# Optimization experiments

Measured on AMD Instinct MI355X. Metric: run time of the kernel, lower is better.

## Reference

```python
import jax, jax.numpy as jnp
import numpy as np

B, T, IN, H, OUT = 32, 1024, 256, 768, 128


def setup_inputs() -> dict:
    key = jax.random.key(0)
    ks = jax.random.split(key, 11)
    s = 0.05
    return {
        "x": jax.random.normal(ks[0], (B, T, IN), dtype=jnp.float32),
        "W_ih0": jax.random.normal(ks[1], (4 * H, IN), dtype=jnp.float32) * s,
        "W_hh0": jax.random.normal(ks[2], (4 * H, H), dtype=jnp.float32) * s,
        "b_ih0": jax.random.normal(ks[3], (4 * H,), dtype=jnp.float32) * s,
        "b_hh0": jax.random.normal(ks[4], (4 * H,), dtype=jnp.float32) * s,
        "W_ih1": jax.random.normal(ks[5], (4 * H, H), dtype=jnp.float32) * s,
        "W_hh1": jax.random.normal(ks[6], (4 * H, H), dtype=jnp.float32) * s,
        "b_ih1": jax.random.normal(ks[7], (4 * H,), dtype=jnp.float32) * s,
        "b_hh1": jax.random.normal(ks[8], (4 * H,), dtype=jnp.float32) * s,
        "W_lin": jax.random.normal(ks[9], (OUT, H), dtype=jnp.float32) * s,
        "b_lin": jax.random.normal(ks[10], (OUT,), dtype=jnp.float32) * s,
    }


def _lstm_layer(x_btd, W_ih, W_hh, b_ih, b_hh):
    # Input-side GEMM for all timesteps at once: [B,T,4H]
    xg = jnp.einsum("btd,gd->btg", x_btd, W_ih) + b_ih + b_hh
    xg = jnp.swapaxes(xg, 0, 1)  # time-major [T,B,4H]
    h0 = jnp.zeros((x_btd.shape[0], W_hh.shape[1]), x_btd.dtype)

    def step(carry, gx):
        h, c = carry
        g = gx + h @ W_hh.T  # [B,4H]
        i, f, gg, o = jnp.split(g, 4, axis=-1)  # PyTorch gate order i,f,g,o
        i, f, o = jax.nn.sigmoid(i), jax.nn.sigmoid(f), jax.nn.sigmoid(o)
        c = f * c + i * jnp.tanh(gg)
        h = o * jnp.tanh(c)
        return (h, c), h

    _, hs = jax.lax.scan(step, (h0, h0), xg)  # hs: [T,B,H]
    return jnp.swapaxes(hs, 0, 1)  # [B,T,H]


def reference(x, W_ih0, W_hh0, b_ih0, b_hh0, W_ih1, W_hh1, b_ih1, b_hh1, W_lin, b_lin):
    h1 = _lstm_layer(x, W_ih0, W_hh0, b_ih0, b_hh0)
    h2 = _lstm_layer(h1, W_ih1, W_hh1, b_ih1, b_hh1)  # eval mode: inter-layer dropout off
    return jnp.einsum("bth,oh->bto", h2, W_lin) + b_lin
```

## Files before the change

### kernel.cpp

```cpp
#include <hip/hip_runtime.h>

#define Tt    1024
#define INF   256
#define Hh    768
#define OUTF  128

#define NWG_L0  48
#define NWG_L1  48
#define NWG_LIN 2
#define NWG     (NWG_L0 + NWG_L1 + NWG_LIN)
#define NTHR    1024

typedef unsigned int       u32;
typedef unsigned long long u64;
typedef unsigned short     u16;
typedef __attribute__((ext_vector_type(8))) short bf16x8;
typedef __attribute__((ext_vector_type(4))) float f32x4;

#define PROG_OFF 0
#define HA_OFF   16384
#define HB_OFF   (HA_OFF + 3*49152)
#define WS_BYTES (HB_OFF + 3*49152)
#define HPS      24576

#define ASTR_B 1552
#define RSLAB  272
#define RROW   17

__device__ __forceinline__ float sigf(float v){ return 1.0f/(1.0f+__expf(-v)); }
__device__ __forceinline__ float tanhfast(float x){
    const float cx = fminf(fmaxf(x, -15.f), 15.f);
    const float e  = __expf(2.f * cx);
    return (e - 1.f) / (e + 1.f);
}
__device__ __forceinline__ u16 f2bf(float f){
    u32 u = __float_as_uint(f);
    return (u16)((u + 0x7fffu + ((u>>16)&1u)) >> 16);
}
__device__ __forceinline__ void st32ws(u16* p, u32 v){
    __hip_atomic_store((u32*)p, v, __ATOMIC_RELAXED, __HIP_MEMORY_SCOPE_AGENT);
}
__device__ __forceinline__ u32 ldu32(const u32* p){
    return __hip_atomic_load(p, __ATOMIC_RELAXED, __HIP_MEMORY_SCOPE_AGENT);
}
__device__ __forceinline__ void stu32(u32* p, u32 v){
    __hip_atomic_store(p, v, __ATOMIC_RELAXED, __HIP_MEMORY_SCOPE_AGENT);
}
__device__ __forceinline__ void ld16x3(const u16* p0, const u16* p1, const u16* p2,
                                       f32x4& r0, f32x4& r1, f32x4& r2){
    asm volatile(
        "global_load_dwordx4 %0, %3, off sc0 sc1\n\t"
        "global_load_dwordx4 %1, %4, off sc0 sc1\n\t"
        "global_load_dwordx4 %2, %5, off sc0 sc1\n\t"
        "s_waitcnt vmcnt(0)"
        : "=&v"(r0), "=&v"(r1), "=&v"(r2)
        : "v"(p0), "v"(p1), "v"(p2)
        : "memory");
}
__device__ __forceinline__ void ld16x6(const u16* p0, const u16* p1, const u16* p2,
                                       const u16* p3, const u16* p4, const u16* p5,
                                       f32x4& r0, f32x4& r1, f32x4& r2,
                                       f32x4& r3, f32x4& r4, f32x4& r5){
    asm volatile(
        "global_load_dwordx4 %0, %6, off sc0 sc1\n\t"
        "global_load_dwordx4 %1, %7, off sc0 sc1\n\t"
        "global_load_dwordx4 %2, %8, off sc0 sc1\n\t"
        "global_load_dwordx4 %3, %9, off sc0 sc1\n\t"
        "global_load_dwordx4 %4, %10, off sc0 sc1\n\t"
        "global_load_dwordx4 %5, %11, off sc0 sc1\n\t"
        "s_waitcnt vmcnt(0)"
        : "=&v"(r0), "=&v"(r1), "=&v"(r2), "=&v"(r3), "=&v"(r4), "=&v"(r5)
        : "v"(p0), "v"(p1), "v"(p2), "v"(p3), "v"(p4), "v"(p5)
        : "memory");
}

__device__ __forceinline__ void waitlines(u32* prog, int base, int cnt, u32 thr, int lane){
    bool ok = (lane >= cnt);
    int guard = 0;
    while (guard < (1 << 24)) {
        if (!ok) ok = (ldu32(prog + (base + lane) * 32) >= thr);
        if (__ballot(ok) == ~0ull) break;
        __builtin_amdgcn_s_sleep(1);
        ++guard;
    }
}

__global__ void prologue(char* ws){
    int i = blockIdx.x * 256 + threadIdx.x;
    if (i < WS_BYTES / 4)
        __hip_atomic_store(((u32*)ws) + i, 0u, __ATOMIC_RELAXED, __HIP_MEMORY_SCOPE_AGENT);
}

__device__ __forceinline__ bf16x8 load8w(const float* p){
    float4 v0 = *(const float4*)(p);
    float4 v1 = *(const float4*)(p + 4);
    bf16x8 r;
    r[0]=(short)f2bf(v0.x); r[1]=(short)f2bf(v0.y); r[2]=(short)f2bf(v0.z); r[3]=(short)f2bf(v0.w);
    r[4]=(short)f2bf(v1.x); r[5]=(short)f2bf(v1.y); r[6]=(short)f2bf(v1.z); r[7]=(short)f2bf(v1.w);
    return r;
}

__global__ __launch_bounds__(NTHR) void lstm_persist(
    const float* __restrict__ x,
    const float* __restrict__ Wih0, const float* __restrict__ Whh0,
    const float* __restrict__ bih0, const float* __restrict__ bhh0,
    const float* __restrict__ Wih1, const float* __restrict__ Whh1,
    const float* __restrict__ bih1, const float* __restrict__ bhh1,
    const float* __restrict__ Wlin, const float* __restrict__ blin,
    float* __restrict__ out, char* ws)
{
    u32* prog = (u32*)(ws + PROG_OFF);
    u16* hA   = (u16*)(ws + HA_OFF);
    u16* hB   = (u16*)(ws + HB_OFF);

    const int wg  = blockIdx.x;
    const int tid = threadIdx.x;

    __shared__ __align__(16) char smem[49664];
    char*  actb = smem;
    float* red  = (float*)smem;

    const int lane = tid & 63, w = tid >> 6;
    const int quad = lane >> 4, nl = lane & 15;
    const int nt = w >> 2, ks = w & 3;
    const int b3 = tid >> 5, q = tid & 31;

    const int role  = (wg < NWG_L0) ? 0 : ((wg < NWG_L0 + NWG_L1) ? 1 : 2);
    const int jbase = (role == 0) ? wg * 16 : ((role == 1) ? (wg - NWG_L0) * 16 : 0);
    const int obase = (role == 2) ? (wg - NWG_L0 - NWG_L1) * 64 : 0;

    bf16x8 bfr[12];
    if (role == 0) {
        const int grow = nt * Hh + jbase + nl;
        #pragma unroll
        for (int fi = 0; fi < 8; ++fi) {
            const int c = fi >> 2, fc = fi & 3;
            const int ka = c * 512 + ks * 128 + fc * 32 + quad * 8;
            const float* p = (ka < 256) ? (Wih0 + (size_t)grow * 256 + ka)
                                        : (Whh0 + (size_t)grow * 768 + (ka - 256));
            bfr[fi] = load8w(p);
        }
    } else if (role == 1) {
        const int grow = nt * Hh + jbase + nl;
        #pragma unroll
        for (int fi = 0; fi < 12; ++fi) {
            const int c = fi / 6, fc = fi % 6;
            const int ka = c * 768 + ks * 192 + fc * 32 + quad * 8;
            const float* p = (ka < 768) ? (Wih1 + (size_t)grow * 768 + ka)
                                        : (Whh1 + (size_t)grow * 768 + (ka - 768));
            bfr[fi] = load8w(p);
        }
    } else {
        const int row = obase + nt * 16 + nl;
        #pragma unroll
        for (int fi = 0; fi < 6; ++fi) {
            const int ka = ks * 192 + fi * 32 + quad * 8;
            bfr[fi] = load8w(Wlin + (size_t)row * 768 + ka);
        }
    }

    float ba0=0,ba1=0,ba2=0,ba3=0, bb0=0,bb1=0,bb2=0,bb3=0, creg0=0, creg1=0;
    float bl0 = 0.f, bl1 = 0.f;
    if (role < 2 && tid < 256) {
        const int jg0 = jbase + 2 * (tid >> 5), jg1 = jg0 + 1;
        const float* bi = (role == 0) ? bih0 : bih1;
        const float* bh = (role == 0) ? bhh0 : bhh1;
        ba0 = bi[jg0]        + bh[jg0];        bb0 = bi[jg1]        + bh[jg1];
        ba1 = bi[768 + jg0]  + bh[768 + jg0];  bb1 = bi[768 + jg1]  + bh[768 + jg1];
        ba2 = bi[1536 + jg0] + bh[1536 + jg0]; bb2 = bi[1536 + jg1] + bh[1536 + jg1];
        ba3 = bi[2304 + jg0] + bh[2304 + jg0]; bb3 = bi[2304 + jg1] + bh[2304 + jg1];
    }
    if (role == 2) {
        bl0 = blin[obase + (tid >> 5)];
        bl1 = blin[obase + 32 + (tid >> 5)];
    }

    for (int s = 0; s < Tt + 2; ++s) {
        const bool active = (role == 0) ? (s < Tt)
                          : (role == 1) ? (s >= 1 && s <= Tt)
                          :               (s >= 2);
        const int par_wA = s % 3;
        const int par_rA = (s + 2) % 3;
        const int par_wB = (s + 2) % 3;
        const int par_rB = (s + 1) % 3;

        if (active && w == 0) {
            if (role == 0) {
                if (s >= 1) waitlines(prog, 0, 48, (u32)s, lane);
                if (s >= 2) waitlines(prog, 48, 48, (u32)(s - 1), lane);
            } else if (role == 1) {
                waitlines(prog, 48, 48, (u32)s, lane);
                {
                    const u32 thr2 = (lane < 48) ? (u32)s : (u32)(s - 1);
                    const int idx  = (lane < 48) ? lane : (96 + (lane - 48));
                    bool ok = (lane >= 50);
                    int guard = 0;
                    while (guard < (1 << 24)) {
                        if (!ok) ok = (ldu32(prog + idx * 32) >= thr2);
                        if (__ballot(ok) == ~0ull) break;
                        __builtin_amdgcn_s_sleep(1);
                        ++guard;
                    }
                }
            } else {
                waitlines(prog, 48, 48, (u32)s, lane);
            }
        }
        __syncthreads();

        if (active) {
            f32x4 acc0 = {0.f,0.f,0.f,0.f}, acc1 = {0.f,0.f,0.f,0.f};

            if (role == 0) {
                const float* xs = x + ((size_t)b3 * Tt + s) * INF + q * 8;
                const float4 v0 = *(const float4*)xs;
                const float4 v1 = *(const float4*)(xs + 4);
                const u16* hp = hA + (size_t)par_rA * HPS + b3 * 768;
                f32x4 h0, h1, h2;
                ld16x3(hp + q * 8, hp + 256 + q * 8, hp + 512 + q * 8, h0, h1, h2);
                {
                    uint4 xv;
                    xv.x = (u32)f2bf(v0.x) | ((u32)f2bf(v0.y) << 16);
                    xv.y = (u32)f2bf(v0.z) | ((u32)f2bf(v0.w) << 16);
                    xv.z = (u32)f2bf(v1.x) | ((u32)f2bf(v1.y) << 16);
                    xv.w = (u32)f2bf(v1.z) | ((u32)f2bf(v1.w) << 16);
                    *(uint4*)(actb + b3 * ASTR_B + q * 16) = xv;
                    *(f32x4*)(actb + b3 * ASTR_B + 512 + q * 16) = h0;
                }
                __syncthreads();
                #pragma unroll
                for (int fc = 0; fc < 4; ++fc) {
                    const int koff = ks * 128 + fc * 32 + quad * 8;
                    bf16x8 a0 = *(const bf16x8*)(actb + nl * ASTR_B + koff * 2);
                    bf16x8 a1 = *(const bf16x8*)(actb + (16 + nl) * ASTR_B + koff * 2);
                    acc0 = __builtin_amdgcn_mfma_f32_16x16x32_bf16(a0, bfr[fc], acc0, 0, 0, 0);
                    acc1 = __builtin_amdgcn_mfma_f32_16x16x32_bf16(a1, bfr[fc], acc1, 0, 0, 0);
                }
                __syncthreads();
                *(f32x4*)(actb + b3 * ASTR_B + q * 16)       = h1;
                *(f32x4*)(actb + b3 * ASTR_B + 512 + q * 16) = h2;
                __syncthreads();
                #pragma unroll
                for (int fc = 0; fc < 4; ++fc) {
                    const int koff = ks * 128 + fc * 32 + quad * 8;
                    bf16x8 a0 = *(const bf16x8*)(actb + nl * ASTR_B + koff * 2);
                    bf16x8 a1 = *(const bf16x8*)(actb + (16 + nl) * ASTR_B + koff * 2);
                    acc0 = __builtin_amdgcn_mfma_f32_16x16x32_bf16(a0, bfr[4 + fc], acc0, 0, 0, 0);
                    acc1 = __builtin_amdgcn_mfma_f32_16x16x32_bf16(a1, bfr[4 + fc], acc1, 0, 0, 0);
                }
                __syncthreads();
            } else if (role == 1) {
                const u16* pA = hA + (size_t)par_rA * HPS + b3 * 768;
                const u16* pB = hB + (size_t)par_rB * HPS + b3 * 768;
                f32x4 a0, a1, a2, bq0, bq1, bq2;
                ld16x6(pA + q * 8, pA + 256 + q * 8, pA + 512 + q * 8,
                       pB + q * 8, pB + 256 + q * 8, pB + 512 + q * 8,
                       a0, a1, a2, bq0, bq1, bq2);
                *(f32x4*)(actb + b3 * ASTR_B + q * 16)        = a0;
                *(f32x4*)(actb + b3 * ASTR_B + 512 + q * 16)  = a1;
                *(f32x4*)(actb + b3 * ASTR_B + 1024 + q * 16) = a2;
                __syncthreads();
                #pragma unroll
                for (int fc = 0; fc < 6; ++fc) {
                    const int koff = ks * 192 + fc * 32 + quad * 8;
                    bf16x8 f0 = *(const bf16x8*)(actb + nl * ASTR_B + koff * 2);
                    bf16x8 f1 = *(const bf16x8*)(actb + (16 + nl) * ASTR_B + koff * 2);
                    acc0 = __builtin_amdgcn_mfma_f32_16x16x32_bf16(f0, bfr[fc], acc0, 0, 0, 0);
                    acc1 = __builtin_amdgcn_mfma_f32_16x16x32_bf16(f1, bfr[fc], acc1, 0, 0, 0);
                }
                __syncthreads();
                *(f32x4*)(actb + b3 * ASTR_B + q * 16)        = bq0;
                *(f32x4*)(actb + b3 * ASTR_B + 512 + q * 16)  = bq1;
                *(f32x4*)(actb + b3 * ASTR_B + 1024 + q * 16) = bq2;
                __syncthreads();
                #pragma unroll
                for (int fc = 0; fc < 6; ++fc) {
                    const int koff = ks * 192 + fc * 32 + quad * 8;
                    bf16x8 f0 = *(const bf16x8*)(actb + nl * ASTR_B + koff * 2);
                    bf16x8 f1 = *(const bf16x8*)(actb + (16 + nl) * ASTR_B + koff * 2);
                    acc0 = __builtin_amdgcn_mfma_f32_16x16x32_bf16(f0, bfr[6 + fc], acc0, 0, 0, 0);
                    acc1 = __builtin_amdgcn_mfma_f32_16x16x32_bf16(f1, bfr[6 + fc], acc1, 0, 0, 0);
                }
                __syncthreads();
            } else {
                const u16* pB = hB + (size_t)par_rB * HPS + b3 * 768;
                f32x4 bq0, bq1, bq2;
                ld16x3(pB + q * 8, pB + 256 + q * 8, pB + 512 + q * 8, bq0, bq1, bq2);
                *(f32x4*)(actb + b3 * ASTR_B + q * 16)        = bq0;
                *(f32x4*)(actb + b3 * ASTR_B + 512 + q * 16)  = bq1;
                *(f32x4*)(actb + b3 * ASTR_B + 1024 + q * 16) = bq2;
                __syncthreads();
                #pragma unroll
                for (int fc = 0; fc < 6; ++fc) {
                    const int koff = ks * 192 + fc * 32 + quad * 8;
                    bf16x8 f0 = *(const bf16x8*)(actb + nl * ASTR_B + koff * 2);
                    bf16x8 f1 = *(const bf16x8*)(actb + (16 + nl) * ASTR_B + koff * 2);
                    acc0 = __builtin_amdgcn_mfma_f32_16x16x32_bf16(f0, bfr[fc], acc0, 0, 0, 0);
                    acc1 = __builtin_amdgcn_mfma_f32_16x16x32_bf16(f1, bfr[fc], acc1, 0, 0, 0);
                }
                __syncthreads();
            }

            *(f32x4*)(red + (size_t)((nt * 2 + 0) * 4 + ks) * RSLAB + nl * RROW + quad * 4) = acc0;
            *(f32x4*)(red + (size_t)((nt * 2 + 1) * 4 + ks) * RSLAB + nl * RROW + quad * 4) = acc1;
            __syncthreads();

            if (role == 2) {
                const int r2 = tid >> 5, bb = tid & 31;
                const int mtr = bb >> 4, mr = bb & 15;
                const int nt0 = r2 >> 4, nr0 = r2 & 15;
                const int nt1 = (r2 + 32) >> 4, nr1 = (r2 + 32) & 15;
                float s0 = 0.f, s1 = 0.f;
                #pragma unroll
                for (int k2 = 0; k2 < 4; ++k2) {
                    s0 += red[(size_t)((nt0 * 2 + mtr) * 4 + k2) * RSLAB + nr0 * RROW + mr];
                    s1 += red[(size_t)((nt1 * 2 + mtr) * 4 + k2) * RSLAB + nr1 * RROW + mr];
                }
                const int v = s - 2;
                float* o = out + ((size_t)bb * Tt + v) * OUTF + obase;
                o[r2]      = s0 + bl0;
                o[32 + r2] = s1 + bl1;
            } else if (tid < 256) {
                const int jj = tid >> 5, b2 = tid & 31;
                const int mt = b2 >> 4, mr = b2 & 15;
                const int j0 = 2 * jj, j1 = 2 * jj + 1;
                float p0a=0,p1a=0,p2a=0,p3a=0, p0b=0,p1b=0,p2b=0,p3b=0;
                #pragma unroll
                for (int k2 = 0; k2 < 4; ++k2) {
                    p0a += red[(size_t)((0 * 2 + mt) * 4 + k2) * RSLAB + j0 * RROW + mr];
                    p1a += red[(size_t)((1 * 2 + mt) * 4 + k2) * RSLAB + j0 * RROW + mr];
                    p2a += red[(size_t)((2 * 2 + mt) * 4 + k2) * RSLAB + j0 * RROW + mr];
                    p3a += red[(size_t)((3 * 2 + mt) * 4 + k2) * RSLAB + j0 * RROW + mr];
                    p0b += red[(size_t)((0 * 2 + mt) * 4 + k2) * RSLAB + j1 * RROW + mr];
                    p1b += red[(size_t)((1 * 2 + mt) * 4 + k2) * RSLAB + j1 * RROW + mr];
                    p2b += red[(size_t)((2 * 2 + mt) * 4 + k2) * RSLAB + j1 * RROW + mr];
                    p3b += red[(size_t)((3 * 2 + mt) * 4 + k2) * RSLAB + j1 * RROW + mr];
                }
                const float ig0 = sigf(ba0 + p0a), fg0 = sigf(ba1 + p1a);
                const float gv0 = tanhfast(ba2 + p2a), og0 = sigf(ba3 + p3a);
                creg0 = fg0 * creg0 + ig0 * gv0;
                const float h0 = og0 * tanhfast(creg0);
                const float ig1 = sigf(bb0 + p0b), fg1 = sigf(bb1 + p1b);
                const float gv1 = tanhfast(bb2 + p2b), og1 = sigf(bb3 + p3b);
                creg1 = fg1 * creg1 + ig1 * gv1;
                const float h1 = og1 * tanhfast(creg1);
                u16* dst = (role == 0) ? (hA + (size_t)par_wA * HPS)
                                       : (hB + (size_t)par_wB * HPS);
                st32ws(dst + b2 * 768 + jbase + j0, (u32)f2bf(h0) | ((u32)f2bf(h1) << 16));
            }
        }

        __syncthreads();
        if (tid == 0) stu32(prog + wg * 32, (u32)(s + 1));
    }
}

extern "C" void kernel_launch(void* const* d_in, const int* in_sizes, int n_in,
                              void* d_out, int out_size, void* d_ws, size_t ws_size,
                              hipStream_t stream)
{
    const float* x    = (const float*)d_in[0];
    const float* Wih0 = (const float*)d_in[1];
    const float* Whh0 = (const float*)d_in[2];
    const float* bih0 = (const float*)d_in[3];
    const float* bhh0 = (const float*)d_in[4];
    const float* Wih1 = (const float*)d_in[5];
    const float* Whh1 = (const float*)d_in[6];
    const float* bih1 = (const float*)d_in[7];
    const float* bhh1 = (const float*)d_in[8];
    const float* Wlin = (const float*)d_in[9];
    const float* blin = (const float*)d_in[10];
    float* out = (float*)d_out;
    char*  ws  = (char*)d_ws;

    hipLaunchKernelGGL(prologue, dim3(304), dim3(256), 0, stream, ws);
    hipLaunchKernelGGL(lstm_persist, dim3(NWG), dim3(NTHR), 0, stream,
                       x, Wih0, Whh0, bih0, bhh0,
                       Wih1, Whh1, bih1, bhh1,
                       Wlin, blin, out, ws);
}
```

Measured before the change: 6.240 ms.

## Stage full activation row in LDS and use dedicated poller wave for step sync

Each timestep's whole concatenated input (x and h, or hA and hB) is now staged into a larger dynamically sized LDS buffer in a single pass. This removes the two-half load/MFMA phases and their extra __syncthreads. A dedicated wave (w==14) polls the cross-workgroup progress flags for both dependencies at once and releases the other waves through an LDS ready counter. The gate nonlinearity is moved to a single wave holding the cell state. The change trades a larger LDS footprint and spin-waiting waves for fewer barriers and shorter per-step latency on the serial recurrence.

```diff
diff --git a/kernel.cpp b/kernel.cpp
--- a/kernel.cpp
+++ b/kernel.cpp
@@ -10,22 +10,29 @@
 #define NWG_LIN 2
 #define NWG     (NWG_L0 + NWG_L1 + NWG_LIN)
 #define NTHR    1024
+#define NIT     (Tt + 2)
 
 typedef unsigned int       u32;
-typedef unsigned long long u64;
 typedef unsigned short     u16;
 typedef __attribute__((ext_vector_type(8))) short bf16x8;
 typedef __attribute__((ext_vector_type(4))) float f32x4;
 
 #define PROG_OFF 0
+#define HPS      24576
 #define HA_OFF   16384
-#define HB_OFF   (HA_OFF + 3*49152)
-#define WS_BYTES (HB_OFF + 3*49152)
-#define HPS      24576
-
-#define ASTR_B 1552
-#define RSLAB  272
-#define RROW   17
+#define HB_OFF   (HA_OFF + 3 * 49152)
+#define WS_BYTES (HB_OFF + 3 * 49152)
+
+#define AST0   2064
+#define AST1   3088
+#define AST2   1552
+#define ACT0_B (32 * AST0)
+#define ACT1_B (32 * AST1)
+#define ACT2_B (32 * AST2)
+#define RSLAB  320
+#define RCOL   20
+#define RED_B  (32 * RSLAB * 4)
+#define LDS_B  (ACT1_B + RED_B)
 
 __device__ __forceinline__ float sigf(float v){ return 1.0f/(1.0f+__expf(-v)); }
 __device__ __forceinline__ float tanhfast(float x){
@@ -57,32 +64,42 @@
         : "v"(p0), "v"(p1), "v"(p2)
         : "memory");
 }
-__device__ __forceinline__ void ld16x6(const u16* p0, const u16* p1, const u16* p2,
+__device__ __forceinline__ void ld16x5(const u16* p0, const u16* p1, const u16* p2,
+                                       const u16* p3, const u16* p4,
+                                       f32x4& r0, f32x4& r1, f32x4& r2,
+                                       f32x4& r3, f32x4& r4){
+    asm volatile(
+        "global_load_dwordx4 %0, %5, off sc0 sc1\n\t"
+        "global_load_dwordx4 %1, %6, off sc0 sc1\n\t"
+        "global_load_dwordx4 %2, %7, off sc0 sc1\n\t"
+        "global_load_dwordx4 %3, %8, off sc0 sc1\n\t"
+        "global_load_dwordx4 %4, %9, off sc0 sc1\n\t"
+        "s_waitcnt vmcnt(0)"
+        : "=&v"(r0), "=&v"(r1), "=&v"(r2), "=&v"(r3), "=&v"(r4)
+        : "v"(p0), "v"(p1), "v"(p2), "v"(p3), "v"(p4)
+        : "memory");
+}
+__device__ __forceinline__ void ld16x7(const u16* p0, const u16* p1, const u16* p2,
                                        const u16* p3, const u16* p4, const u16* p5,
-                                       f32x4& r0, f32x4& r1, f32x4& r2,
-                                       f32x4& r3, f32x4& r4, f32x4& r5){
+                                       const u16* p6,
+                                       f32x4& r0, f32x4& r1, f32x4& r2, f32x4& r3,
+                                       f32x4& r4, f32x4& r5, f32x4& r6){
     asm volatile(
-        "global_load_dwordx4 %0, %6, off sc0 sc1\n\t"
-        "global_load_dwordx4 %1, %7, off sc0 sc1\n\t"
-        "global_load_dwordx4 %2, %8, off sc0 sc1\n\t"
-        "global_load_dwordx4 %3, %9, off sc0 sc1\n\t"
-        "global_load_dwordx4 %4, %10, off sc0 sc1\n\t"
-        "global_load_dwordx4 %5, %11, off sc0 sc1\n\t"
+        "global_load_dwordx4 %0, %7, off sc0 sc1\n\t"
+        "global_load_dwordx4 %1, %8, off sc0 sc1\n\t"
+        "global_load_dwordx4 %2, %9, off sc0 sc1\n\t"
+        "global_load_dwordx4 %3, %10, off sc0 sc1\n\t"
+        "global_load_dwordx4 %4, %11, off sc0 sc1\n\t"
+        "global_load_dwordx4 %5, %12, off sc0 sc1\n\t"
+        "global_load_dwordx4 %6, %13, off sc0 sc1\n\t"
         "s_waitcnt vmcnt(0)"
-        : "=&v"(r0), "=&v"(r1), "=&v"(r2), "=&v"(r3), "=&v"(r4), "=&v"(r5)
-        : "v"(p0), "v"(p1), "v"(p2), "v"(p3), "v"(p4), "v"(p5)
+        : "=&v"(r0), "=&v"(r1), "=&v"(r2), "=&v"(r3),
+          "=&v"(r4), "=&v"(r5), "=&v"(r6)
+        : "v"(p0), "v"(p1), "v"(p2), "v"(p3), "v"(p4), "v"(p5), "v"(p6)
         : "memory");
 }
-
-__device__ __forceinline__ void waitlines(u32* prog, int base, int cnt, u32 thr, int lane){
-    bool ok = (lane >= cnt);
-    int guard = 0;
-    while (guard < (1 << 24)) {
-        if (!ok) ok = (ldu32(prog + (base + lane) * 32) >= thr);
-        if (__ballot(ok) == ~0ull) break;
-        __builtin_amdgcn_s_sleep(1);
-        ++guard;
-    }
+__device__ __forceinline__ void waitvm(){
+    asm volatile("s_waitcnt vmcnt(0)" ::: "memory");
 }
 
 __global__ void prologue(char* ws){
@@ -116,26 +133,26 @@
     const int wg  = blockIdx.x;
     const int tid = threadIdx.x;
 
-    __shared__ __align__(16) char smem[49664];
-    char*  actb = smem;
-    float* red  = (float*)smem;
+    extern __shared__ __align__(16) char smem[];
+    __shared__ u32 rdy;
 
     const int lane = tid & 63, w = tid >> 6;
     const int quad = lane >> 4, nl = lane & 15;
     const int nt = w >> 2, ks = w & 3;
-    const int b3 = tid >> 5, q = tid & 31;
 
     const int role  = (wg < NWG_L0) ? 0 : ((wg < NWG_L0 + NWG_L1) ? 1 : 2);
     const int jbase = (role == 0) ? wg * 16 : ((role == 1) ? (wg - NWG_L0) * 16 : 0);
     const int obase = (role == 2) ? (wg - NWG_L0 - NWG_L1) * 64 : 0;
+
+    char*  actb = smem;
+    float* red  = (float*)(smem + ((role == 0) ? ACT0_B : (role == 1) ? ACT1_B : ACT2_B));
 
     bf16x8 bfr[12];
     if (role == 0) {
         const int grow = nt * Hh + jbase + nl;
         #pragma unroll
         for (int fi = 0; fi < 8; ++fi) {
-            const int c = fi >> 2, fc = fi & 3;
-            const int ka = c * 512 + ks * 128 + fc * 32 + quad * 8;
+            const int ka = ks * 256 + fi * 32 + quad * 8;
             const float* p = (ka < 256) ? (Wih0 + (size_t)grow * 256 + ka)
                                         : (Whh0 + (size_t)grow * 768 + (ka - 256));
             bfr[fi] = load8w(p);
@@ -144,8 +161,7 @@
         const int grow = nt * Hh + jbase + nl;
         #pragma unroll
         for (int fi = 0; fi < 12; ++fi) {
-            const int c = fi / 6, fc = fi % 6;
-            const int ka = c * 768 + ks * 192 + fc * 32 + quad * 8;
+            const int ka = ks * 384 + fi * 32 + quad * 8;
             const float* p = (ka < 768) ? (Wih1 + (size_t)grow * 768 + ka)
                                         : (Whh1 + (size_t)grow * 768 + (ka - 768));
             bfr[fi] = load8w(p);
@@ -159,199 +175,240 @@
         }
     }
 
-    float ba0=0,ba1=0,ba2=0,ba3=0, bb0=0,bb1=0,bb2=0,bb3=0, creg0=0, creg1=0;
-    float bl0 = 0.f, bl1 = 0.f;
-    if (role < 2 && tid < 256) {
-        const int jg0 = jbase + 2 * (tid >> 5), jg1 = jg0 + 1;
+    float ba[4] = {0,0,0,0}, bb[4] = {0,0,0,0};
+    float ca[4] = {0,0,0,0}, cb[4] = {0,0,0,0};
+    if (role < 2 && w == 15) {
         const float* bi = (role == 0) ? bih0 : bih1;
         const float* bh = (role == 0) ? bhh0 : bhh1;
-        ba0 = bi[jg0]        + bh[jg0];        bb0 = bi[jg1]        + bh[jg1];
-        ba1 = bi[768 + jg0]  + bh[768 + jg0];  bb1 = bi[768 + jg1]  + bh[768 + jg1];
-        ba2 = bi[1536 + jg0] + bh[1536 + jg0]; bb2 = bi[1536 + jg1] + bh[1536 + jg1];
-        ba3 = bi[2304 + jg0] + bh[2304 + jg0]; bb3 = bi[2304 + jg1] + bh[2304 + jg1];
+        const int jg0 = jbase + 2 * (lane >> 3), jg1 = jg0 + 1;
+        #pragma unroll
+        for (int g = 0; g < 4; ++g) {
+            ba[g] = bi[g * 768 + jg0] + bh[g * 768 + jg0];
+            bb[g] = bi[g * 768 + jg1] + bh[g * 768 + jg1];
+        }
     }
+    float bl0 = 0.f, bl1 = 0.f;
     if (role == 2) {
-        bl0 = blin[obase + (tid >> 5)];
-        bl1 = blin[obase + 32 + (tid >> 5)];
+        bl0 = blin[obase + (tid & 31)];
+        bl1 = blin[obase + 32 + (tid & 31)];
     }
 
-    for (int s = 0; s < Tt + 2; ++s) {
-        const bool active = (role == 0) ? (s < Tt)
-                          : (role == 1) ? (s >= 1 && s <= Tt)
-                          :               (s >= 2);
+    if (tid == 0) __hip_atomic_store(&rdy, 0u, __ATOMIC_RELAXED, __HIP_MEMORY_SCOPE_WORKGROUP);
+    __syncthreads();
+
+    for (int s = 0; s < NIT; ++s) {
         const int par_wA = s % 3;
         const int par_rA = (s + 2) % 3;
         const int par_wB = (s + 2) % 3;
         const int par_rB = (s + 1) % 3;
-
-        if (active && w == 0) {
+        const bool active = (role == 0) ? (s < Tt)
+                          : (role == 1) ? (s >= 1 && s <= Tt)
+                          :               (s >= 2);
+        if (active) {
+            if (w == 14) {
+                int ia = -1, ib = -1; u32 ta = 0, tb = 0;
+                if (role == 0) {
+                    if (lane < 48) {
+                        ia = lane; ta = (u32)s;
+                        if (s >= 3) { ib = 48 + lane; tb = (u32)(s-1); }
+                    }
+                } else if (role == 1) {
+                    if (lane < 48) {
+                        ia = lane; ta = (u32)s;
+                        ib = 48 + lane;
+                        tb = (s >= 2) ? (u32)s : 0u;
+                    } else if (lane < 50) {
+                        ib = 48 + lane;
+                        tb = (s >= 4) ? (u32)(s-1) : 0u;
+                    }
+                } else {
+                    if (lane < 48) { ia = 48 + lane; ta = (u32)s; }
+                }
+                int guard = 0;
+                while (guard < (1 << 24)) {
+                    const bool o1 = (ia < 0) || (ldu32(prog + ia * 32) >= ta);
+                    const bool o2 = (ib < 0) || (ldu32(prog + ib * 32) >= tb);
+                    if (__ballot(o1 && o2) == ~0ull) break;
+                    __builtin_amdgcn_s_sleep(1); ++guard;
+                }
+                if (lane == 0)
+                    __hip_atomic_store(&rdy, (u32)(s + 1), __ATOMIC_RELAXED, __HIP_MEMORY_SCOPE_WORKGROUP);
+            } else {
+                int guard = 0;
+                while (guard < (1 << 24) &&
+                       __hip_atomic_load(&rdy, __ATOMIC_RELAXED, __HIP_MEMORY_SCOPE_WORKGROUP) < (u32)(s + 1)) {
+                    __builtin_amdgcn_s_sleep(1); ++guard;
+                }
+            }
+
             if (role == 0) {
-                if (s >= 1) waitlines(prog, 0, 48, (u32)s, lane);
-                if (s >= 2) waitlines(prog, 48, 48, (u32)(s - 1), lane);
+                if (tid < 960) {
+                    const u16* hsrc = hA + (size_t)par_rA * HPS;
+                    int Gv[5]; u32 la[5]; bool vx[5], vh[5]; const u16* pp[5];
+                    #pragma unroll
+                    for (int u = 0; u < 5; ++u) {
+                        Gv[u] = (u < 4) ? (u * 960 + tid) : (3840 + tid);
+                        const bool val = (u < 4) || (tid < 256);
+                        const int row = Gv[u] >> 7, c = Gv[u] & 127;
+                        la[u] = (u32)(row * AST0 + c * 16);
+                        vx[u] = val && (c < 32);
+                        vh[u] = val && (c >= 32);
+                        pp[u] = vh[u] ? (hsrc + (size_t)row * 768 + (size_t)(c - 32) * 8)
+                                      : hsrc;
+                    }
+                    #pragma unroll
+                    for (int u = 0; u < 5; ++u) if (vx[u]) {
+                        const int row = Gv[u] >> 7, c = Gv[u] & 127;
+                        const float* xs = x + ((size_t)row * Tt + s) * INF + c * 8;
+                        const float4 v0 = ((const float4*)xs)[0];
+                        const float4 v1 = ((const float4*)xs)[1];
+                        uint4 a;
+                        a.x = (u32)f2bf(v0.x) | ((u32)f2bf(v0.y) << 16);
+                        a.y = (u32)f2bf(v0.z) | ((u32)f2bf(v0.w) << 16);
+                        a.z = (u32)f2bf(v1.x) | ((u32)f2bf(v1.y) << 16);
+                        a.w = (u32)f2bf(v1.z) | ((u32)f2bf(v1.w) << 16);
+                        *(uint4*)(actb + la[u]) = a;
+                    }
+                    f32x4 h0, h1, h2, h3, h4;
+                    ld16x5(pp[0], pp[1], pp[2], pp[3], pp[4], h0, h1, h2, h3, h4);
+                    if (vh[0]) *(f32x4*)(actb + la[0]) = h0;
+                    if (vh[1]) *(f32x4*)(actb + la[1]) = h1;
+                    if (vh[2]) *(f32x4*)(actb + la[2]) = h2;
+                    if (vh[3]) *(f32x4*)(actb + la[3]) = h3;
+                    if (vh[4]) *(f32x4*)(actb + la[4]) = h4;
+                }
             } else if (role == 1) {
-                waitlines(prog, 48, 48, (u32)s, lane);
-                {
-                    const u32 thr2 = (lane < 48) ? (u32)s : (u32)(s - 1);
-                    const int idx  = (lane < 48) ? lane : (96 + (lane - 48));
-                    bool ok = (lane >= 50);
-                    int guard = 0;
-                    while (guard < (1 << 24)) {
-                        if (!ok) ok = (ldu32(prog + idx * 32) >= thr2);
-                        if (__ballot(ok) == ~0ull) break;
-                        __builtin_amdgcn_s_sleep(1);
-                        ++guard;
-                    }
+                if (tid < 960) {
+                    const u16* pA = hA + (size_t)par_rA * HPS;
+                    const u16* pB = hB + (size_t)par_rB * HPS;
+                    u32 la[7]; const u16* pp[7]; bool v6 = (tid < 384);
+                    #pragma unroll
+                    for (int u = 0; u < 7; ++u) {
+                        const int G = (u < 6) ? (u * 960 + tid) : (5760 + tid);
+                        const bool val = (u < 6) || v6;
+                        const int row = G / 192, c = G - row * 192;
+                        la[u] = (u32)(row * AST1 + c * 16);
+                        pp[u] = !val ? pA
+                              : (c < 96) ? (pA + (size_t)row * 768 + (size_t)c * 8)
+                                         : (pB + (size_t)row * 768 + (size_t)(c - 96) * 8);
+                    }
+                    f32x4 h0, h1, h2, h3, h4, h5, h6;
+                    ld16x7(pp[0], pp[1], pp[2], pp[3], pp[4], pp[5], pp[6],
+                           h0, h1, h2, h3, h4, h5, h6);
+                    *(f32x4*)(actb + la[0]) = h0;
+                    *(f32x4*)(actb + la[1]) = h1;
+                    *(f32x4*)(actb + la[2]) = h2;
+                    *(f32x4*)(actb + la[3]) = h3;
+                    *(f32x4*)(actb + la[4]) = h4;
+                    *(f32x4*)(actb + la[5]) = h5;
+                    if (v6) *(f32x4*)(actb + la[6]) = h6;
                 }
             } else {
-                waitlines(prog, 48, 48, (u32)s, lane);
+                const u16* pB = hB + (size_t)par_rB * HPS;
+                u32 la[3]; const u16* pp[3];
+                #pragma unroll
+                for (int u = 0; u < 3; ++u) {
+                    const int G = u * 1024 + tid;
+                    const int row = G / 96, c = G - row * 96;
+                    la[u] = (u32)(row * AST2 + c * 16);
+                    pp[u] = pB + (size_t)row * 768 + (size_t)c * 8;
+                }
+                f32x4 h0, h1, h2;
+                ld16x3(pp[0], pp[1], pp[2], h0, h1, h2);
+                *(f32x4*)(actb + la[0]) = h0;
+                *(f32x4*)(actb + la[1]) = h1;
+                *(f32x4*)(actb + la[2]) = h2;
+            }
+            __syncthreads();
+
+            f32x4 acc0 = {0.f,0.f,0.f,0.f}, acc1 = {0.f,0.f,0.f,0.f};
+            if (role == 0) {
+                #pragma unroll
+                for (int fc = 0; fc < 8; ++fc) {
+                    const int kb = (ks * 256 + fc * 32 + quad * 8) * 2;
+                    bf16x8 a0 = *(const bf16x8*)(actb + nl * AST0 + kb);
+                    bf16x8 a1 = *(const bf16x8*)(actb + (16 + nl) * AST0 + kb);
+                    acc0 = __builtin_amdgcn_mfma_f32_16x16x32_bf16(a0, bfr[fc], acc0, 0, 0, 0);
+                    acc1 = __builtin_amdgcn_mfma_f32_16x16x32_bf16(a1, bfr[fc], acc1, 0, 0, 0);
+                }
+            } else if (role == 1) {
+                #pragma unroll
+                for (int fc = 0; fc < 12; ++fc) {
+                    const int kb = (ks * 384 + fc * 32 + quad * 8) * 2;
+                    bf16x8 a0 = *(const bf16x8*)(actb + nl * AST1 + kb);
+                    bf16x8 a1 = *(const bf16x8*)(actb + (16 + nl) * AST1 + kb);
+                    acc0 = __builtin_amdgcn_mfma_f32_16x16x32_bf16(a0, bfr[fc], acc0, 0, 0, 0);
+                    acc1 = __builtin_amdgcn_mfma_f32_16x16x32_bf16(a1, bfr[fc], acc1, 0, 0, 0);
+                }
+            } else {
+                #pragma unroll
+                for (int fc = 0; fc < 6; ++fc) {
+                    const int kb = (ks * 192 + fc * 32 + quad * 8) * 2;
+                    bf16x8 a0 = *(const bf16x8*)(actb + nl * AST2 + kb);
+                    bf16x8 a1 = *(const bf16x8*)(actb + (16 + nl) * AST2 + kb);
+                    acc0 = __builtin_amdgcn_mfma_f32_16x16x32_bf16(a0, bfr[fc], acc0, 0, 0, 0);
+                    acc1 = __builtin_amdgcn_mfma_f32_16x16x32_bf16(a1, bfr[fc], acc1, 0, 0, 0);
+                }
+            }
+            *(f32x4*)&red[(size_t)((nt * 2 + 0) * 4 + ks) * RSLAB + nl * RCOL + quad * 4] = acc0;
+            *(f32x4*)&red[(size_t)((nt * 2 + 1) * 4 + ks) * RSLAB + nl * RCOL + quad * 4] = acc1;
+            __syncthreads();
+
+            if (role == 2) {
+                if (tid == 0) stu32(prog + wg * 32, (u32)(s + 1));
+                const int v = s - 2;
+                const int orow = tid >> 5, oc2 = tid & 31;
+                const int mh = orow >> 4, r16 = orow & 15;
+                const int nt0 = oc2 >> 4, n0 = oc2 & 15;
+                float s0 = bl0, s1 = bl1;
+                #pragma unroll
+                for (int k2 = 0; k2 < 4; ++k2) {
+                    s0 += red[(size_t)((nt0 * 2 + mh) * 4 + k2) * RSLAB + n0 * RCOL + r16];
+                    s1 += red[(size_t)(((nt0 + 2) * 2 + mh) * 4 + k2) * RSLAB + n0 * RCOL + r16];
+                }
+                float* o = out + ((size_t)orow * Tt + v) * OUTF + obase;
+                o[oc2]      = s0;
+                o[32 + oc2] = s1;
+            } else if (w == 15) {
+                const int jp = lane >> 3, rg = lane & 7;
+                const int mh = rg >> 2, rr = 4 * (rg & 3);
+                f32x4 pga[4], pgb[4];
+                #pragma unroll
+                for (int g = 0; g < 4; ++g) {
+                    const int sb0 = (g * 2 + mh) * 4;
+                    f32x4 sa = {0.f,0.f,0.f,0.f}, sb = {0.f,0.f,0.f,0.f};
+                    #pragma unroll
+                    for (int k2 = 0; k2 < 4; ++k2) {
+                        sa += *(const f32x4*)&red[(size_t)(sb0 + k2) * RSLAB + (2 * jp) * RCOL + rr];
+                        sb += *(const f32x4*)&red[(size_t)(sb0 + k2) * RSLAB + (2 * jp + 1) * RCOL + rr];
+                    }
+                    pga[g] = sa; pgb[g] = sb;
+                }
+                u16* dst = (role == 0) ? (hA + (size_t)par_wA * HPS)
+                                       : (hB + (size_t)par_wB * HPS);
+                #pragma unroll
+                for (int i = 0; i < 4; ++i) {
+                    const float ig0 = sigf(ba[0] + pga[0][i]);
+                    const float fg0 = sigf(ba[1] + pga[1][i]);
+                    const float gv0 = tanhfast(ba[2] + pga[2][i]);
+                    const float og0 = sigf(ba[3] + pga[3][i]);
+                    ca[i] = fg0 * ca[i] + ig0 * gv0;
+                    const float h0 = og0 * tanhfast(ca[i]);
+                    const float ig1 = sigf(bb[0] + pgb[0][i]);
+                    const float fg1 = sigf(bb[1] + pgb[1][i]);
+                    const float gv1 = tanhfast(bb[2] + pgb[2][i]);
+                    const float og1 = sigf(bb[3] + pgb[3][i]);
+                    cb[i] = fg1 * cb[i] + ig1 * gv1;
+                    const float h1 = og1 * tanhfast(cb[i]);
+                    st32ws(dst + (size_t)(4 * rg + i) * 768 + jbase + 2 * jp,
+                           (u32)f2bf(h0) | ((u32)f2bf(h1) << 16));
+                }
+                waitvm();
+                if (lane == 0)
+                    __hip_atomic_store(prog + wg * 32, (u32)(s + 1),
+                                       __ATOMIC_RELEASE, __HIP_MEMORY_SCOPE_AGENT);
             }
         }
-        __syncthreads();
-
-        if (active) {
-            f32x4 acc0 = {0.f,0.f,0.f,0.f}, acc1 = {0.f,0.f,0.f,0.f};
-
-            if (role == 0) {
-                const float* xs = x + ((size_t)b3 * Tt + s) * INF + q * 8;
-                const float4 v0 = *(const float4*)xs;
-                const float4 v1 = *(const float4*)(xs + 4);
-                const u16* hp = hA + (size_t)par_rA * HPS + b3 * 768;
-                f32x4 h0, h1, h2;
-                ld16x3(hp + q * 8, hp + 256 + q * 8, hp + 512 + q * 8, h0, h1, h2);
-                {
-                    uint4 xv;
-                    xv.x = (u32)f2bf(v0.x) | ((u32)f2bf(v0.y) << 16);
-                    xv.y = (u32)f2bf(v0.z) | ((u32)f2bf(v0.w) << 16);
-                    xv.z = (u32)f2bf(v1.x) | ((u32)f2bf(v1.y) << 16);
-                    xv.w = (u32)f2bf(v1.z) | ((u32)f2bf(v1.w) << 16);
-                    *(uint4*)(actb + b3 * ASTR_B + q * 16) = xv;
-                    *(f32x4*)(actb + b3 * ASTR_B + 512 + q * 16) = h0;
-                }
-                __syncthreads();
-                #pragma unroll
-                for (int fc = 0; fc < 4; ++fc) {
-                    const int koff = ks * 128 + fc * 32 + quad * 8;
-                    bf16x8 a0 = *(const bf16x8*)(actb + nl * ASTR_B + koff * 2);
-                    bf16x8 a1 = *(const bf16x8*)(actb + (16 + nl) * ASTR_B + koff * 2);
-                    acc0 = __builtin_amdgcn_mfma_f32_16x16x32_bf16(a0, bfr[fc], acc0, 0, 0, 0);
-                    acc1 = __builtin_amdgcn_mfma_f32_16x16x32_bf16(a1, bfr[fc], acc1, 0, 0, 0);
-                }
-                __syncthreads();
-                *(f32x4*)(actb + b3 * ASTR_B + q * 16)       = h1;
-                *(f32x4*)(actb + b3 * ASTR_B + 512 + q * 16) = h2;
-                __syncthreads();
-                #pragma unroll
-                for (int fc = 0; fc < 4; ++fc) {
-                    const int koff = ks * 128 + fc * 32 + quad * 8;
-                    bf16x8 a0 = *(const bf16x8*)(actb + nl * ASTR_B + koff * 2);
-                    bf16x8 a1 = *(const bf16x8*)(actb + (16 + nl) * ASTR_B + koff * 2);
-                    acc0 = __builtin_amdgcn_mfma_f32_16x16x32_bf16(a0, bfr[4 + fc], acc0, 0, 0, 0);
-                    acc1 = __builtin_amdgcn_mfma_f32_16x16x32_bf16(a1, bfr[4 + fc], acc1, 0, 0, 0);
-                }
-                __syncthreads();
-            } else if (role == 1) {
-                const u16* pA = hA + (size_t)par_rA * HPS + b3 * 768;
-                const u16* pB = hB + (size_t)par_rB * HPS + b3 * 768;
-                f32x4 a0, a1, a2, bq0, bq1, bq2;
-                ld16x6(pA + q * 8, pA + 256 + q * 8, pA + 512 + q * 8,
-                       pB + q * 8, pB + 256 + q * 8, pB + 512 + q * 8,
-                       a0, a1, a2, bq0, bq1, bq2);
-                *(f32x4*)(actb + b3 * ASTR_B + q * 16)        = a0;
-                *(f32x4*)(actb + b3 * ASTR_B + 512 + q * 16)  = a1;
-                *(f32x4*)(actb + b3 * ASTR_B + 1024 + q * 16) = a2;
-                __syncthreads();
-                #pragma unroll
-                for (int fc = 0; fc < 6; ++fc) {
-                    const int koff = ks * 192 + fc * 32 + quad * 8;
-                    bf16x8 f0 = *(const bf16x8*)(actb + nl * ASTR_B + koff * 2);
-                    bf16x8 f1 = *(const bf16x8*)(actb + (16 + nl) * ASTR_B + koff * 2);
-                    acc0 = __builtin_amdgcn_mfma_f32_16x16x32_bf16(f0, bfr[fc], acc0, 0, 0, 0);
-                    acc1 = __builtin_amdgcn_mfma_f32_16x16x32_bf16(f1, bfr[fc], acc1, 0, 0, 0);
-                }
-                __syncthreads();
-                *(f32x4*)(actb + b3 * ASTR_B + q * 16)        = bq0;
-                *(f32x4*)(actb + b3 * ASTR_B + 512 + q * 16)  = bq1;
-                *(f32x4*)(actb + b3 * ASTR_B + 1024 + q * 16) = bq2;
-                __syncthreads();
-                #pragma unroll
-                for (int fc = 0; fc < 6; ++fc) {
-                    const int koff = ks * 192 + fc * 32 + quad * 8;
-                    bf16x8 f0 = *(const bf16x8*)(actb + nl * ASTR_B + koff * 2);
-                    bf16x8 f1 = *(const bf16x8*)(actb + (16 + nl) * ASTR_B + koff * 2);
-                    acc0 = __builtin_amdgcn_mfma_f32_16x16x32_bf16(f0, bfr[6 + fc], acc0, 0, 0, 0);
-                    acc1 = __builtin_amdgcn_mfma_f32_16x16x32_bf16(f1, bfr[6 + fc], acc1, 0, 0, 0);
-                }
-                __syncthreads();
-            } else {
-                const u16* pB = hB + (size_t)par_rB * HPS + b3 * 768;
-                f32x4 bq0, bq1, bq2;
-                ld16x3(pB + q * 8, pB + 256 + q * 8, pB + 512 + q * 8, bq0, bq1, bq2);
-                *(f32x4*)(actb + b3 * ASTR_B + q * 16)        = bq0;
-                *(f32x4*)(actb + b3 * ASTR_B + 512 + q * 16)  = bq1;
-                *(f32x4*)(actb + b3 * ASTR_B + 1024 + q * 16) = bq2;
-                __syncthreads();
-                #pragma unroll
-                for (int fc = 0; fc < 6; ++fc) {
-                    const int koff = ks * 192 + fc * 32 + quad * 8;
-                    bf16x8 f0 = *(const bf16x8*)(actb + nl * ASTR_B + koff * 2);
-                    bf16x8 f1 = *(const bf16x8*)(actb + (16 + nl) * ASTR_B + koff * 2);
-                    acc0 = __builtin_amdgcn_mfma_f32_16x16x32_bf16(f0, bfr[fc], acc0, 0, 0, 0);
-                    acc1 = __builtin_amdgcn_mfma_f32_16x16x32_bf16(f1, bfr[fc], acc1, 0, 0, 0);
-                }
-                __syncthreads();
-            }
-
-            *(f32x4*)(red + (size_t)((nt * 2 + 0) * 4 + ks) * RSLAB + nl * RROW + quad * 4) = acc0;
-            *(f32x4*)(red + (size_t)((nt * 2 + 1) * 4 + ks) * RSLAB + nl * RROW + quad * 4) = acc1;
-            __syncthreads();
-
-            if (role == 2) {
-                const int r2 = tid >> 5, bb = tid & 31;
-                const int mtr = bb >> 4, mr = bb & 15;
-                const int nt0 = r2 >> 4, nr0 = r2 & 15;
-                const int nt1 = (r2 + 32) >> 4, nr1 = (r2 + 32) & 15;
-                float s0 = 0.f, s1 = 0.f;
-                #pragma unroll
-                for (int k2 = 0; k2 < 4; ++k2) {
-                    s0 += red[(size_t)((nt0 * 2 + mtr) * 4 + k2) * RSLAB + nr0 * RROW + mr];
-                    s1 += red[(size_t)((nt1 * 2 + mtr) * 4 + k2) * RSLAB + nr1 * RROW + mr];
-                }
-                const int v = s - 2;
-                float* o = out + ((size_t)bb * Tt + v) * OUTF + obase;
-                o[r2]      = s0 + bl0;
-                o[32 + r2] = s1 + bl1;
-            } else if (tid < 256) {
-                const int jj = tid >> 5, b2 = tid & 31;
-                const int mt = b2 >> 4, mr = b2 & 15;
-                const int j0 = 2 * jj, j1 = 2 * jj + 1;
-                float p0a=0,p1a=0,p2a=0,p3a=0, p0b=0,p1b=0,p2b=0,p3b=0;
-                #pragma unroll
-                for (int k2 = 0; k2 < 4; ++k2) {
-                    p0a += red[(size_t)((0 * 2 + mt) * 4 + k2) * RSLAB + j0 * RROW + mr];
-                    p1a += red[(size_t)((1 * 2 + mt) * 4 + k2) * RSLAB + j0 * RROW + mr];
-                    p2a += red[(size_t)((2 * 2 + mt) * 4 + k2) * RSLAB + j0 * RROW + mr];
-                    p3a += red[(size_t)((3 * 2 + mt) * 4 + k2) * RSLAB + j0 * RROW + mr];
-                    p0b += red[(size_t)((0 * 2 + mt) * 4 + k2) * RSLAB + j1 * RROW + mr];
-                    p1b += red[(size_t)((1 * 2 + mt) * 4 + k2) * RSLAB + j1 * RROW + mr];
-                    p2b += red[(size_t)((2 * 2 + mt) * 4 + k2) * RSLAB + j1 * RROW + mr];
-                    p3b += red[(size_t)((3 * 2 + mt) * 4 + k2) * RSLAB + j1 * RROW + mr];
-                }
-                const float ig0 = sigf(ba0 + p0a), fg0 = sigf(ba1 + p1a);
-                const float gv0 = tanhfast(ba2 + p2a), og0 = sigf(ba3 + p3a);
-                creg0 = fg0 * creg0 + ig0 * gv0;
-                const float h0 = og0 * tanhfast(creg0);
-                const float ig1 = sigf(bb0 + p0b), fg1 = sigf(bb1 + p1b);
-                const float gv1 = tanhfast(bb2 + p2b), og1 = sigf(bb3 + p3b);
-                creg1 = fg1 * creg1 + ig1 * gv1;
-                const float h1 = og1 * tanhfast(creg1);
-                u16* dst = (role == 0) ? (hA + (size_t)par_wA * HPS)
-                                       : (hB + (size_t)par_wB * HPS);
-                st32ws(dst + b2 * 768 + jbase + j0, (u32)f2bf(h0) | ((u32)f2bf(h1) << 16));
-            }
-        }
-
-        __syncthreads();
-        if (tid == 0) stu32(prog + wg * 32, (u32)(s + 1));
     }
 }
 
@@ -373,8 +430,15 @@
     float* out = (float*)d_out;
     char*  ws  = (char*)d_ws;
 
+    static bool attr_done = false;
+    if (!attr_done) {
+        hipFuncSetAttribute((const void*)lstm_persist,
+                            hipFuncAttributeMaxDynamicSharedMemorySize, 160 * 1024);
+        attr_done = true;
+    }
+
     hipLaunchKernelGGL(prologue, dim3(304), dim3(256), 0, stream, ws);
-    hipLaunchKernelGGL(lstm_persist, dim3(NWG), dim3(NTHR), 0, stream,
+    hipLaunchKernelGGL(lstm_persist, dim3(NWG), dim3(NTHR), LDS_B, stream,
                        x, Wih0, Whh0, bih0, bhh0,
                        Wih1, Whh1, bih1, bhh1,
                        Wlin, blin, out, ws);
```

Result: slower. 12.91 ms (+107.0%).
